# Performance work log

Measured on AMD Instinct MI355X. Metric: run time of the kernel, lower is better.

## Reference

```python
import jax, jax.numpy as jnp
import numpy as np

B, S, E, H, F, V = 4, 2048, 1024, 16, 4096, 32000
D = E // H  # head_dim = 64
LN_EPS = 1e-5


def layer_norm(x, g, b):
    mu = jnp.mean(x, axis=-1, keepdims=True)
    var = jnp.mean(jnp.square(x - mu), axis=-1, keepdims=True)
    return (x - mu) * jax.lax.rsqrt(var + LN_EPS) * g + b


def setup_inputs() -> dict:
    key = jax.random.key(0)
    ks = jax.random.split(key, 12)
    s = 0.02
    return {
        "input_ids": jax.random.randint(ks[0], (B, S), 0, V),
        "attention_mask": jnp.ones((B, S), dtype=jnp.int32),
        "emb_table": jax.random.normal(ks[1], (V, E), jnp.float32) * s,
        "Wq": jax.random.normal(ks[2], (E, E), jnp.float32) * s,
        "bq": jnp.zeros((E,), jnp.float32),
        "Wk": jax.random.normal(ks[3], (E, E), jnp.float32) * s,
        "bk": jnp.zeros((E,), jnp.float32),
        "Wv": jax.random.normal(ks[4], (E, E), jnp.float32) * s,
        "bv": jnp.zeros((E,), jnp.float32),
        "Wo": jax.random.normal(ks[5], (E, E), jnp.float32) * s,
        "bo": jnp.zeros((E,), jnp.float32),
        "ln_g": jnp.ones((E,), jnp.float32),
        "ln_b": jnp.zeros((E,), jnp.float32),
        "W1": jax.random.normal(ks[6], (E, F), jnp.float32) * s,
        "b1": jnp.zeros((F,), jnp.float32),
        "W2": jax.random.normal(ks[7], (F, E), jnp.float32) * s,
        "b2": jnp.zeros((E,), jnp.float32),
        "Wp": jax.random.normal(ks[8], (E, 3), jnp.float32) * s,
        "bp": jnp.zeros((3,), jnp.float32),
    }


def reference(input_ids, attention_mask, emb_table, Wq, bq, Wk, bk, Wv, bv,
              Wo, bo, ln_g, ln_b, W1, b1, W2, b2, Wp, bp):
    b, s = input_ids.shape
    x = emb_table[input_ids]                                  # [B,S,E]
    q = (x @ Wq + bq).reshape(b, s, H, D).transpose(0, 2, 1, 3)  # [B,H,S,D]
    k = (x @ Wk + bk).reshape(b, s, H, D).transpose(0, 2, 1, 3)
    v = (x @ Wv + bv).reshape(b, s, H, D).transpose(0, 2, 1, 3)
    scores = jnp.einsum('bhqd,bhkd->bhqk', q, k) / jnp.sqrt(jnp.float32(D))
    mask = attention_mask[:, None, None, :]                   # [B,1,1,S]
    scores = jnp.where(mask == 0, -jnp.inf, scores)
    attn = jax.nn.softmax(scores, axis=-1)
    ctx = jnp.einsum('bhqk,bhkd->bhqd', attn, v)              # [B,H,S,D]
    ctx = ctx.transpose(0, 2, 1, 3).reshape(b, s, E)
    ctx = ctx @ Wo + bo
    h = layer_norm(ctx + x, ln_g, ln_b)
    ff = jax.nn.gelu(h @ W1 + b1, approximate=False) @ W2 + b2
    logits = ff @ Wp + bp                                     # [B,S,3]
    return logits.mean(axis=1)                                # [B,3]
```

## Files before the change

### kernel.cpp

```cpp
#include <hip/hip_runtime.h>
#include <hip/hip_bf16.h>
#include <math.h>

#define BB 4
#define SS 2048
#define EE 1024
#define HH 16
#define DD 64
#define FF 4096

typedef unsigned short u16;
typedef unsigned int u32;
typedef __bf16 bf16x8 __attribute__((ext_vector_type(8)));
typedef float f32x4 __attribute__((ext_vector_type(4)));

static __device__ __forceinline__ float gelu_exact(float v){
  return 0.5f * v * (1.0f + erff(v * 0.70710678118654752f));
}

static __device__ __forceinline__ u16 f2bf(float f){
  union { float f; u32 u; } x; x.f = f;
  u32 r = x.u + 0x7FFFu + ((x.u >> 16) & 1u);
  return (u16)(r >> 16);
}
static __device__ __forceinline__ u16 f2bf_hw(float f){
  union { __bf16 b; u16 u; } c; c.b = (__bf16)f; return c.u;
}
static __device__ __forceinline__ void unpack2(u32 u, float& lo, float& hi){
  union { u32 u; float f; } a, b;
  a.u = u << 16; b.u = u & 0xFFFF0000u;
  lo = a.f; hi = b.f;
}

#define GLOAD_LDS16(g, l) \
  __builtin_amdgcn_global_load_lds((const __attribute__((address_space(1))) void*)(g), \
      (__attribute__((address_space(3))) void*)(l), 16, 0, 0)

__global__ __launch_bounds__(256) void embed_kernel(const int* __restrict__ ids,
    const float* __restrict__ emb, float* __restrict__ xf, u16* __restrict__ xbf){
  int row = blockIdx.x;
  int id  = ids[row];
  float4 v = ((const float4*)(emb + (size_t)id * EE))[threadIdx.x];
  ((float4*)(xf + (size_t)row * EE))[threadIdx.x] = v;
  ushort4 u; u.x = f2bf(v.x); u.y = f2bf(v.y); u.z = f2bf(v.z); u.w = f2bf(v.w);
  ((ushort4*)(xbf + (size_t)row * EE))[threadIdx.x] = u;
}

__global__ __launch_bounds__(256) void prep_weights(const float* __restrict__ Wq,
    const float* __restrict__ Wk, const float* __restrict__ Wv,
    const float* __restrict__ Wo, const float* __restrict__ W1, u16* __restrict__ WT){
  __shared__ float tile[32][33];
  int bid = blockIdx.x;
  const float* W; u16* dst; int N, n0, k0;
  if (bid < 4096){
    W = W1; dst = WT + (size_t)4 * EE * EE; N = FF;
    n0 = (bid & 127) * 32; k0 = (bid >> 7) * 32;
  } else {
    int idx = bid - 4096;
    int which = idx >> 10, t = idx & 1023;
    W = (which == 0) ? Wq : (which == 1) ? Wk : (which == 2) ? Wv : Wo;
    dst = WT + (size_t)which * EE * EE; N = EE;
    n0 = (t & 31) * 32; k0 = (t >> 5) * 32;
  }
  int tx = threadIdx.x & 31, ty = threadIdx.x >> 5;
  #pragma unroll
  for (int i = 0; i < 4; i++)
    tile[ty + 8*i][tx] = W[(size_t)(k0 + ty + 8*i) * N + n0 + tx];
  __syncthreads();
  #pragma unroll
  for (int i = 0; i < 4; i++)
    dst[(size_t)(n0 + ty + 8*i) * EE + k0 + tx] = f2bf(tile[tx][ty + 8*i]);
}

template<int MODE>
__global__ __launch_bounds__(256) void gemm_mfma(const u16* __restrict__ A,
    const u16* __restrict__ WT, const float* __restrict__ bias,
    const float* __restrict__ biasB, const float* __restrict__ biasC,
    u16* __restrict__ C, float* __restrict__ gsum, int M, int N, int K){
  __shared__ __attribute__((aligned(16))) u16 As[2][128 * 32];
  __shared__ __attribute__((aligned(16))) u16 Bs[2][128 * 32];

  const int tid = threadIdx.x;
  const int l = tid & 63, w = tid >> 6;
  const int lm = l & 15, lq = l >> 4;
  const int wm = (w >> 1) * 64, wn = (w & 1) * 64;

  const int nwg = gridDim.x * gridDim.y;
  const int bid = blockIdx.y * gridDim.x + blockIdx.x;
  const int q8  = nwg >> 3;
  const int lin = (bid & 7) * q8 + (bid >> 3);
  const int bx  = lin % gridDim.x;
  const int by  = lin / gridDim.x;
  const int r0 = by * 128, c0 = bx * 128;

  const int srow0 = w * 32 + (l >> 2);
  const int scol  = (l & 3) * 8;
  const u16* Ab = A  + (size_t)(r0 + srow0) * K + scol;
  const u16* Bb = WT + (size_t)(c0 + srow0) * K + scol;
  const int sbase = (w * 2) * 512;

  f32x4 acc[4][4];
  const f32x4 zero = {0.f, 0.f, 0.f, 0.f};
  #pragma unroll
  for (int mi = 0; mi < 4; mi++)
    #pragma unroll
    for (int ni = 0; ni < 4; ni++) acc[mi][ni] = zero;

  GLOAD_LDS16(Ab,                  &As[0][sbase]);
  GLOAD_LDS16(Ab + (size_t)16 * K, &As[0][sbase + 512]);
  GLOAD_LDS16(Bb,                  &Bs[0][sbase]);
  GLOAD_LDS16(Bb + (size_t)16 * K, &Bs[0][sbase + 512]);
  __syncthreads();

  int p = 0;
  for (int k0 = 0; k0 < K; k0 += 32){
    if (k0 + 32 < K){
      const int pn = p ^ 1;
      GLOAD_LDS16(Ab + k0 + 32,                   &As[pn][sbase]);
      GLOAD_LDS16(Ab + (size_t)16 * K + k0 + 32,  &As[pn][sbase + 512]);
      GLOAD_LDS16(Bb + k0 + 32,                   &Bs[pn][sbase]);
      GLOAD_LDS16(Bb + (size_t)16 * K + k0 + 32,  &Bs[pn][sbase + 512]);
    }

    bf16x8 af[4], bfr[4];
    #pragma unroll
    for (int mi = 0; mi < 4; mi++)
      af[mi] = *(const bf16x8*)&As[p][(wm + mi*16 + lm) * 32 + lq * 8];
    #pragma unroll
    for (int ni = 0; ni < 4; ni++)
      bfr[ni] = *(const bf16x8*)&Bs[p][(wn + ni*16 + lm) * 32 + lq * 8];
    #pragma unroll
    for (int mi = 0; mi < 4; mi++)
      #pragma unroll
      for (int ni = 0; ni < 4; ni++)
        acc[mi][ni] = __builtin_amdgcn_mfma_f32_16x16x32_bf16(af[mi], bfr[ni], acc[mi][ni], 0, 0, 0);

    __syncthreads();
    p ^= 1;
  }

  if constexpr (MODE == 0){
    #pragma unroll
    for (int ni = 0; ni < 4; ni++){
      int col = c0 + wn + ni*16 + lm;
      float bcol = bias[col];
      #pragma unroll
      for (int mi = 0; mi < 4; mi++){
        #pragma unroll
        for (int r = 0; r < 4; r++){
          int row = r0 + wm + mi*16 + lq*4 + r;
          C[(size_t)row * N + col] = f2bf(acc[mi][ni][r] + bcol);
        }
      }
    }
  } else if constexpr (MODE == 2){
    #pragma unroll
    for (int ni = 0; ni < 4; ni++){
      int col3 = c0 + wn + ni*16 + lm;
      int sel  = col3 >> 10;
      int colm = col3 & 1023;
      const float* bp_ = (sel == 0) ? bias : ((sel == 1) ? biasB : biasC);
      float bcol = bp_[colm];
      u16* dst = C + (size_t)sel * ((size_t)M * N);
      #pragma unroll
      for (int mi = 0; mi < 4; mi++){
        #pragma unroll
        for (int r = 0; r < 4; r++){
          int row = r0 + wm + mi*16 + lq*4 + r;
          dst[(size_t)row * N + colm] = f2bf(acc[mi][ni][r] + bcol);
        }
      }
    }
  } else {
    const int batch = r0 >> 11;
    #pragma unroll
    for (int ni = 0; ni < 4; ni++){
      int col = c0 + wn + ni*16 + lm;
      float bcol = bias[col];
      float cs = 0.f;
      #pragma unroll
      for (int mi = 0; mi < 4; mi++)
        #pragma unroll
        for (int r = 0; r < 4; r++)
          cs += gelu_exact(acc[mi][ni][r] + bcol);
      cs += __shfl_xor(cs, 16, 64);
      cs += __shfl_xor(cs, 32, 64);
      if (lq == 0) atomicAdd(&gsum[(size_t)batch * N + col], cs);
    }
  }
}

__global__ __launch_bounds__(256, 2) void attn_mfma(const u16* __restrict__ q,
    const u16* __restrict__ k, const u16* __restrict__ v,
    const int* __restrict__ mask, u16* __restrict__ ctx){
  const int bid = blockIdx.y * gridDim.x + blockIdx.x;
  const int lin = (bid & 7) * 128 + (bid >> 3);
  const int qb  = lin & 15, bh = lin >> 4;
  const int b = bh >> 4, h = bh & 15;
  const int q0 = qb * 128;
  const int tid = threadIdx.x;
  const int w = tid >> 6, l = tid & 63, lm = l & 15, lq = l >> 4;

  __shared__ __attribute__((aligned(16))) u16 smem[128 * 72];
  __shared__ __attribute__((aligned(16))) float mb[64];
  u16* Kt = smem;
  u16* Vt = smem + 64 * 72;

  bf16x8 aq[2][2];
  #pragma unroll
  for (int mg = 0; mg < 2; mg++){
    const u16* qrow = q + (size_t)(b*SS + q0 + w*32 + mg*16 + lm) * EE + h*DD + lq*8;
    aq[mg][0] = *(const bf16x8*)qrow;
    aq[mg][1] = *(const bf16x8*)(qrow + 32);
  }

  f32x4 occ[2][4];
  const f32x4 zero = {0.f,0.f,0.f,0.f};
  #pragma unroll
  for (int mg = 0; mg < 2; mg++)
    #pragma unroll
    for (int mi = 0; mi < 4; mi++) occ[mg][mi] = zero;
  float l_part[2] = {0.f, 0.f};

  const int kkey = tid >> 2, kc16 = (tid & 3) * 16;
  const u16* kbase = k + (size_t)(b*SS + kkey) * EE + h*DD + kc16;
  const int kp = tid & 31, vd0 = (tid >> 5) * 8;
  const u16* vbase0 = v + (size_t)(b*SS + 2*kp) * EE + h*DD + vd0;
  const u16* vbase1 = vbase0 + EE;

  uint4 kr0 = *(const uint4*)(kbase);
  uint4 kr1 = *(const uint4*)(kbase + 8);
  uint4 vr0 = *(const uint4*)(vbase0);
  uint4 vr1 = *(const uint4*)(vbase1);
  float mreg = 0.f;
  if (tid < 64) mreg = (mask[b*SS + tid] != 0) ? 0.f : -1e30f;

  const float SCALE_LOG2E = 0.125f * 1.4426950408889634f;

  for (int t0 = 0; t0 < SS; t0 += 64){
    *(uint4*)&Kt[kkey*72 + kc16]     = kr0;
    *(uint4*)&Kt[kkey*72 + kc16 + 8] = kr1;
    {
      union { uint4 u; u16 s[8]; } va, vb;
      va.u = vr0; vb.u = vr1;
      #pragma unroll
      for (int i = 0; i < 8; i++){
        u32 pk = (u32)va.s[i] | ((u32)vb.s[i] << 16);
        *(u32*)&Vt[(vd0 + i)*72 + 2*kp] = pk;
      }
    }
    if (tid < 64) mb[tid] = mreg;
    __syncthreads();

    if (t0 + 64 < SS){
      kr0 = *(const uint4*)(kbase + (size_t)(t0 + 64) * EE);
      kr1 = *(const uint4*)(kbase + (size_t)(t0 + 64) * EE + 8);
      vr0 = *(const uint4*)(vbase0 + (size_t)(t0 + 64) * EE);
      vr1 = *(const uint4*)(vbase1 + (size_t)(t0 + 64) * EE);
      if (tid < 64) mreg = (mask[b*SS + t0 + 64 + tid] != 0) ? 0.f : -1e30f;
    }

    bf16x8 pb[2][2];
    #pragma unroll
    for (int mg = 0; mg < 2; mg++){
      float lp = 0.f;
      #pragma unroll
      for (int h2 = 0; h2 < 2; h2++){
        u32 pk[2][2];
        #pragma unroll
        for (int np = 0; np < 2; np++){
          int ni = h2*2 + np;
          bf16x8 kf0 = *(const bf16x8*)&Kt[(ni*16 + lm)*72 + lq*8];
          bf16x8 kf1 = *(const bf16x8*)&Kt[(ni*16 + lm)*72 + 32 + lq*8];
          f32x4 sc = zero;
          __builtin_amdgcn_s_setprio(1);
          sc = __builtin_amdgcn_mfma_f32_16x16x32_bf16(kf0, aq[mg][0], sc, 0, 0, 0);
          sc = __builtin_amdgcn_mfma_f32_16x16x32_bf16(kf1, aq[mg][1], sc, 0, 0, 0);
          __builtin_amdgcn_s_setprio(0);
          f32x4 mbv = *(const f32x4*)&mb[ni*16 + lq*4];
          float p[4];
          #pragma unroll
          for (int r = 0; r < 4; r++){
            float s = fminf(fmaf(sc[r], SCALE_LOG2E, mbv[r]), 80.f);
            p[r] = __builtin_amdgcn_exp2f(s);
            lp += p[r];
          }
          pk[np][0] = (u32)f2bf_hw(p[0]) | ((u32)f2bf_hw(p[1]) << 16);
          pk[np][1] = (u32)f2bf_hw(p[2]) | ((u32)f2bf_hw(p[3]) << 16);
        }
        int srcA = lm + 16*((2*lq)     & 3);
        int srcB = lm + 16*((2*lq + 1) & 3);
        u32 x0 = (u32)__shfl((int)pk[0][0], srcA, 64);
        u32 x1 = (u32)__shfl((int)pk[0][1], srcA, 64);
        u32 x2 = (u32)__shfl((int)pk[0][0], srcB, 64);
        u32 x3 = (u32)__shfl((int)pk[0][1], srcB, 64);
        u32 y0 = (u32)__shfl((int)pk[1][0], srcA, 64);
        u32 y1 = (u32)__shfl((int)pk[1][1], srcA, 64);
        u32 y2 = (u32)__shfl((int)pk[1][0], srcB, 64);
        u32 y3 = (u32)__shfl((int)pk[1][1], srcB, 64);
        bool lo = (lq < 2);
        union { u32 u[4]; bf16x8 v; } pu;
        pu.u[0] = lo ? x0 : y0;
        pu.u[1] = lo ? x1 : y1;
        pu.u[2] = lo ? x2 : y2;
        pu.u[3] = lo ? x3 : y3;
        pb[mg][h2] = pu.v;
      }
      l_part[mg] += lp;
    }

    __builtin_amdgcn_s_setprio(1);
    #pragma unroll
    for (int mi = 0; mi < 4; mi++){
      bf16x8 vb0 = *(const bf16x8*)&Vt[(mi*16 + lm)*72 + lq*8];
      bf16x8 vb1 = *(const bf16x8*)&Vt[(mi*16 + lm)*72 + 32 + lq*8];
      #pragma unroll
      for (int mg = 0; mg < 2; mg++){
        occ[mg][mi] = __builtin_amdgcn_mfma_f32_16x16x32_bf16(vb0, pb[mg][0], occ[mg][mi], 0, 0, 0);
        occ[mg][mi] = __builtin_amdgcn_mfma_f32_16x16x32_bf16(vb1, pb[mg][1], occ[mg][mi], 0, 0, 0);
      }
    }
    __builtin_amdgcn_s_setprio(0);
    __syncthreads();
  }

  #pragma unroll
  for (int mg = 0; mg < 2; mg++){
    float s = l_part[mg];
    s += __shfl_xor(s, 16, 64);
    s += __shfl_xor(s, 32, 64);
    float inv = 1.f / s;
    #pragma unroll
    for (int mi = 0; mi < 4; mi++){
      ushort4 o;
      o.x = f2bf(occ[mg][mi][0] * inv);
      o.y = f2bf(occ[mg][mi][1] * inv);
      o.z = f2bf(occ[mg][mi][2] * inv);
      o.w = f2bf(occ[mg][mi][3] * inv);
      *(ushort4*)&smem[(w*32 + mg*16 + lm)*72 + mi*16 + lq*4] = o;
    }
  }
  __syncthreads();
  {
    const int row = tid >> 1, half = tid & 1;
    u16* dst = ctx + (size_t)(b*SS + q0 + row) * EE + h*DD + half*32;
    const u16* src = &smem[row*72 + half*32];
    #pragma unroll
    for (int jj = 0; jj < 4; jj++)
      *(uint4*)(dst + jj*8) = *(const uint4*)(src + jj*8);
  }
}

__global__ __launch_bounds__(256) void ln_kernel(const u16* __restrict__ c2,
    const float* __restrict__ x, const float* __restrict__ g,
    const float* __restrict__ bta, u16* __restrict__ h){
  int row = blockIdx.x, tid = threadIdx.x;
  uint2 cu = ((const uint2*)(c2 + (size_t)row * EE))[tid];
  float c0,c1,c2f,c3;
  unpack2(cu.x, c0, c1); unpack2(cu.y, c2f, c3);
  float4 xv = ((const float4*)(x + (size_t)row * EE))[tid];
  float4 y = make_float4(c0+xv.x, c1+xv.y, c2f+xv.z, c3+xv.w);
  float s  = y.x + y.y + y.z + y.w;
  float ss = y.x*y.x + y.y*y.y + y.z*y.z + y.w*y.w;
  #pragma unroll
  for (int off=32; off; off>>=1){
    s  += __shfl_xor(s,  off, 64);
    ss += __shfl_xor(ss, off, 64);
  }
  __shared__ float rs[4], rss[4];
  int w = tid >> 6;
  if ((tid & 63) == 0){ rs[w] = s; rss[w] = ss; }
  __syncthreads();
  float tot  = rs[0]+rs[1]+rs[2]+rs[3];
  float tots = rss[0]+rss[1]+rss[2]+rss[3];
  float mu  = tot  * (1.f/EE);
  float var = tots * (1.f/EE) - mu*mu;
  float inv = rsqrtf(var + 1e-5f);
  float4 gv = ((const float4*)g)[tid];
  float4 bv = ((const float4*)bta)[tid];
  ushort4 ou;
  ou.x = f2bf((y.x-mu)*inv*gv.x + bv.x);
  ou.y = f2bf((y.y-mu)*inv*gv.y + bv.y);
  ou.z = f2bf((y.z-mu)*inv*gv.z + bv.z);
  ou.w = f2bf((y.w-mu)*inv*gv.w + bv.w);
  ((ushort4*)(h + (size_t)row * EE))[tid] = ou;
}

__global__ __launch_bounds__(256) void w2wp_kernel(const float* __restrict__ W2,
    const float* __restrict__ Wp, float* __restrict__ W2Wp){
  int f0 = blockIdx.x * 8;
  int tid = threadIdx.x;
  int e0 = tid * 4;
  float wp[4][3];
  #pragma unroll
  for (int t = 0; t < 4; t++)
    #pragma unroll
    for (int j = 0; j < 3; j++) wp[t][j] = Wp[(e0 + t)*3 + j];
  __shared__ float red[3][4];
  for (int i = 0; i < 8; i++){
    int f = f0 + i;
    float4 wv = ((const float4*)(W2 + (size_t)f * EE))[tid];
    float w4[4] = {wv.x, wv.y, wv.z, wv.w};
    float p[3] = {0.f, 0.f, 0.f};
    #pragma unroll
    for (int t = 0; t < 4; t++)
      #pragma unroll
      for (int j = 0; j < 3; j++) p[j] += w4[t] * wp[t][j];
    #pragma unroll
    for (int j = 0; j < 3; j++){
      float sj = p[j];
      #pragma unroll
      for (int off = 32; off; off >>= 1) sj += __shfl_xor(sj, off, 64);
      if ((tid & 63) == 0) red[j][tid >> 6] = sj;
    }
    __syncthreads();
    if (tid < 3) W2Wp[f*3 + tid] = red[tid][0] + red[tid][1] + red[tid][2] + red[tid][3];
    __syncthreads();
  }
}

__global__ __launch_bounds__(256) void out_final(const float* __restrict__ gsum,
    const float* __restrict__ W2Wp, const float* __restrict__ b2,
    const float* __restrict__ Wp, const float* __restrict__ bp, float* __restrict__ out){
  int tid = threadIdx.x;
  float part[4][3];
  #pragma unroll
  for (int b = 0; b < 4; b++)
    #pragma unroll
    for (int j = 0; j < 3; j++) part[b][j] = 0.f;
  for (int f = tid; f < FF; f += 256){
    float w0 = W2Wp[f*3], w1 = W2Wp[f*3+1], w2v = W2Wp[f*3+2];
    #pragma unroll
    for (int b = 0; b < 4; b++){
      float g = gsum[b*FF + f] * (1.f/SS);
      part[b][0] += g * w0; part[b][1] += g * w1; part[b][2] += g * w2v;
    }
  }
  float bb[3] = {0.f, 0.f, 0.f};
  for (int e = tid; e < EE; e += 256){
    float bv = b2[e];
    bb[0] += bv * Wp[e*3]; bb[1] += bv * Wp[e*3+1]; bb[2] += bv * Wp[e*3+2];
  }
  __shared__ float red[15][4];
  int lane = tid & 63, w = tid >> 6;
  #pragma unroll
  for (int b = 0; b < 4; b++)
    #pragma unroll
    for (int j = 0; j < 3; j++){
      float s = part[b][j];
      #pragma unroll
      for (int off = 32; off; off >>= 1) s += __shfl_xor(s, off, 64);
      if (lane == 0) red[b*3 + j][w] = s;
    }
  #pragma unroll
  for (int j = 0; j < 3; j++){
    float s = bb[j];
    #pragma unroll
    for (int off = 32; off; off >>= 1) s += __shfl_xor(s, off, 64);
    if (lane == 0) red[12 + j][w] = s;
  }
  __syncthreads();
  if (tid < 12){
    int j = tid % 3;
    float s  = red[tid][0] + red[tid][1] + red[tid][2] + red[tid][3];
    float bj = red[12+j][0] + red[12+j][1] + red[12+j][2] + red[12+j][3];
    out[tid] = s + bj + bp[j];
  }
}

extern "C" void kernel_launch(void* const* d_in, const int* in_sizes, int n_in,
                              void* d_out, int out_size, void* d_ws, size_t ws_size,
                              hipStream_t stream) {
  const int M = BB * SS;
  const int* ids  = (const int*)d_in[0];
  const int* mask = (const int*)d_in[1];
  const float* emb = (const float*)d_in[2];
  const float* Wq = (const float*)d_in[3];  const float* bq = (const float*)d_in[4];
  const float* Wk = (const float*)d_in[5];  const float* bk = (const float*)d_in[6];
  const float* Wv = (const float*)d_in[7];  const float* bv = (const float*)d_in[8];
  const float* Wo = (const float*)d_in[9];  const float* bo = (const float*)d_in[10];
  const float* lg = (const float*)d_in[11]; const float* lb = (const float*)d_in[12];
  const float* W1 = (const float*)d_in[13]; const float* b1 = (const float*)d_in[14];
  const float* W2 = (const float*)d_in[15]; const float* b2 = (const float*)d_in[16];
  const float* Wp = (const float*)d_in[17]; const float* bp = (const float*)d_in[18];

  char* base = (char*)d_ws;
  const size_t SLOTF = (size_t)M * EE;
  float* xf   = (float*)base;
  u16*  xbf   = (u16*)(base + SLOTF*4);
  u16*  qbf   = (u16*)(base + SLOTF*6);
  u16*  kbf   = (u16*)(base + SLOTF*8);
  u16*  vbf   = (u16*)(base + SLOTF*10);
  u16*  ctxbf = (u16*)(base + SLOTF*12);
  u16*  c2bf  = qbf;
  u16*  hbf   = kbf;
  u16*  WqT   = (u16*)(base + SLOTF*14);
  u16*  W1T   = WqT + (size_t)4*EE*EE;
  float* gsum = (float*)(W1T + (size_t)FF*EE);
  float* w2wp = gsum + BB*FF;

  hipMemsetAsync(gsum, 0, BB*FF*sizeof(float), stream);

  embed_kernel<<<M, 256, 0, stream>>>(ids, emb, xf, xbf);

  prep_weights<<<8192, 256, 0, stream>>>(Wq, Wk, Wv, Wo, W1, WqT);
  w2wp_kernel<<<FF/8, 256, 0, stream>>>(W2, Wp, w2wp);

  gemm_mfma<2><<<dim3(3*EE/128, M/128), 256, 0, stream>>>(
      xbf, WqT, bq, bk, bv, qbf, nullptr, M, EE, EE);

  attn_mfma<<<dim3(SS/128, BB*HH), 256, 0, stream>>>(qbf, kbf, vbf, mask, ctxbf);

  gemm_mfma<0><<<dim3(EE/128, M/128), 256, 0, stream>>>(
      ctxbf, WqT + (size_t)3*EE*EE, bo, nullptr, nullptr, c2bf, nullptr, M, EE, EE);

  ln_kernel<<<M, 256, 0, stream>>>(c2bf, xf, lg, lb, hbf);

  gemm_mfma<1><<<dim3(FF/128, M/128), 256, 0, stream>>>(
      hbf, W1T, b1, nullptr, nullptr, nullptr, gsum, M, FF, EE);

  out_final<<<1, 256, 0, stream>>>(gsum, w2wp, b2, Wp, bp, (float*)d_out);
}
```

Measured before the change: 613.1 us.

## Add 256x256 swizzled pipelined GEMM, precompute mask bias, remove attention P shuffles

Adds a new 512-thread GEMM kernel with 256x256 tiles, 64-wide K steps, XOR-swizzled LDS and a staged prefetch interleaved with MFMA groups, and uses it for the QKV projection and the FFN1+GELU reduction. The larger tiles are meant to raise data reuse per LDS load and cut global traffic, at the cost of more registers and LDS per block and fewer blocks in flight. Attention now reads a precomputed float mask bias from global memory instead of staging it through LDS. It also permutes the V layout in LDS so the probability fragments can feed the second MFMA directly, removing eight cross-lane shuffles per step.

Measured after the change: 593.5 us. -3.2%, faster.

```diff
diff --git a/kernel.cpp b/kernel.cpp
--- a/kernel.cpp
+++ b/kernel.cpp
@@ -35,6 +35,12 @@
 #define GLOAD_LDS16(g, l) \
   __builtin_amdgcn_global_load_lds((const __attribute__((address_space(1))) void*)(g), \
       (__attribute__((address_space(3))) void*)(l), 16, 0, 0)
+
+static __device__ __forceinline__ void blockbar(){
+  asm volatile("" ::: "memory");
+  __builtin_amdgcn_s_barrier();
+  asm volatile("" ::: "memory");
+}
 
 __global__ __launch_bounds__(256) void embed_kernel(const int* __restrict__ ids,
     const float* __restrict__ emb, float* __restrict__ xf, u16* __restrict__ xbf){
@@ -44,6 +50,12 @@
   ((float4*)(xf + (size_t)row * EE))[threadIdx.x] = v;
   ushort4 u; u.x = f2bf(v.x); u.y = f2bf(v.y); u.z = f2bf(v.z); u.w = f2bf(v.w);
   ((ushort4*)(xbf + (size_t)row * EE))[threadIdx.x] = u;
+}
+
+__global__ __launch_bounds__(256) void mask_prep(const int* __restrict__ mask,
+    float* __restrict__ mbias){
+  int i = blockIdx.x * 256 + threadIdx.x;
+  mbias[i] = (mask[i] != 0) ? 0.f : -1e30f;
 }
 
 __global__ __launch_bounds__(256) void prep_weights(const float* __restrict__ Wq,
@@ -121,7 +133,6 @@
       GLOAD_LDS16(Bb + k0 + 32,                   &Bs[pn][sbase]);
       GLOAD_LDS16(Bb + (size_t)16 * K + k0 + 32,  &Bs[pn][sbase + 512]);
     }
-
     bf16x8 af[4], bfr[4];
     #pragma unroll
     for (int mi = 0; mi < 4; mi++)
@@ -134,7 +145,6 @@
       #pragma unroll
       for (int ni = 0; ni < 4; ni++)
         acc[mi][ni] = __builtin_amdgcn_mfma_f32_16x16x32_bf16(af[mi], bfr[ni], acc[mi][ni], 0, 0, 0);
-
     __syncthreads();
     p ^= 1;
   }
@@ -153,7 +163,135 @@
         }
       }
     }
-  } else if constexpr (MODE == 2){
+  }
+}
+
+template<int MODE>
+__global__ __launch_bounds__(512, 2) void gemm256(const u16* __restrict__ A,
+    const u16* __restrict__ WT, const float* __restrict__ bias,
+    const float* __restrict__ biasB, const float* __restrict__ biasC,
+    u16* __restrict__ C, float* __restrict__ gsum, int M, int N, int K){
+  __shared__ __attribute__((aligned(16))) u16 As[2 * 256 * 64];
+  __shared__ __attribute__((aligned(16))) u16 Bs[2 * 256 * 64];
+
+  const int tid = threadIdx.x;
+  const int w = tid >> 6, l = tid & 63;
+  const int lm = l & 15, lq = l >> 4;
+  const int wm = (w >> 2) * 128, wn = (w & 3) * 64;
+
+  const int nwg = gridDim.x * gridDim.y;
+  const int bid = blockIdx.y * gridDim.x + blockIdx.x;
+  const int lin = (bid & 7) * (nwg >> 3) + (bid >> 3);
+  const int bx = lin % gridDim.x, by = lin / gridDim.x;
+  const int r0 = by * 256, c0 = bx * 256;
+
+  const int NT = K >> 6;
+  const int arow = w * 8 + (l >> 3);
+  const int acol = ((l & 7) ^ (l >> 3)) * 8;
+  const u16* Ag = A  + (size_t)(r0 + arow) * K + acol;
+  const u16* Bg = WT + (size_t)(c0 + arow) * K + acol;
+  const int dstw = w * 512;
+
+#define STG_A(p_, kt_, g_) GLOAD_LDS16(Ag + (size_t)((g_)*64) * K + (kt_)*64, &As[(p_)*16384 + (g_)*4096 + dstw])
+#define STG_B(p_, kt_, g_) GLOAD_LDS16(Bg + (size_t)((g_)*64) * K + (kt_)*64, &Bs[(p_)*16384 + (g_)*4096 + dstw])
+
+  const int rsw = (lm & 7) << 3;
+#define RD_A(p_, mi_, kk_) (*(const bf16x8*)&As[(p_)*16384 + (wm + (mi_)*16 + lm)*64 + (((kk_)*32 + lq*8) ^ rsw)])
+#define RD_B(p_, ni_, kk_) (*(const bf16x8*)&Bs[(p_)*16384 + (wn + (ni_)*16 + lm)*64 + (((kk_)*32 + lq*8) ^ rsw)])
+
+  f32x4 acc[8][4];
+  const f32x4 zero = {0.f, 0.f, 0.f, 0.f};
+  #pragma unroll
+  for (int mi = 0; mi < 8; mi++)
+    #pragma unroll
+    for (int ni = 0; ni < 4; ni++) acc[mi][ni] = zero;
+
+  #pragma unroll
+  for (int g = 0; g < 4; g++){ STG_A(0, 0, g); STG_B(0, 0, g); }
+  #pragma unroll
+  for (int g = 0; g < 4; g++){ STG_A(1, 1, g); STG_B(1, 1, g); }
+  asm volatile("s_waitcnt vmcnt(8)" ::: "memory");
+  __builtin_amdgcn_s_barrier();
+  asm volatile("" ::: "memory");
+
+  bf16x8 a0[4][2], a1[4][2], b0[2][2], b1[2][2];
+
+  for (int t = 0; t < NT; ++t){
+    const int p = t & 1;
+    const int s = t + 2;
+    const bool st = (s < NT);
+
+    #pragma unroll
+    for (int mi = 0; mi < 4; mi++){ a0[mi][0] = RD_A(p, mi, 0); a0[mi][1] = RD_A(p, mi, 1); }
+    #pragma unroll
+    for (int ni = 0; ni < 2; ni++){ b0[ni][0] = RD_B(p, ni, 0); b0[ni][1] = RD_B(p, ni, 1); }
+    blockbar();
+    __builtin_amdgcn_s_setprio(1);
+    #pragma unroll
+    for (int kk = 0; kk < 2; kk++)
+      #pragma unroll
+      for (int mi = 0; mi < 4; mi++)
+        #pragma unroll
+        for (int ni = 0; ni < 2; ni++)
+          acc[mi][ni] = __builtin_amdgcn_mfma_f32_16x16x32_bf16(a0[mi][kk], b0[ni][kk], acc[mi][ni], 0, 0, 0);
+    __builtin_amdgcn_s_setprio(0);
+    blockbar();
+
+    #pragma unroll
+    for (int ni = 0; ni < 2; ni++){ b1[ni][0] = RD_B(p, ni + 2, 0); b1[ni][1] = RD_B(p, ni + 2, 1); }
+    if (st){ STG_A(p, s, 0); STG_A(p, s, 2); }
+    blockbar();
+    __builtin_amdgcn_s_setprio(1);
+    #pragma unroll
+    for (int kk = 0; kk < 2; kk++)
+      #pragma unroll
+      for (int mi = 0; mi < 4; mi++)
+        #pragma unroll
+        for (int ni = 0; ni < 2; ni++)
+          acc[mi][ni + 2] = __builtin_amdgcn_mfma_f32_16x16x32_bf16(a0[mi][kk], b1[ni][kk], acc[mi][ni + 2], 0, 0, 0);
+    __builtin_amdgcn_s_setprio(0);
+    blockbar();
+
+    #pragma unroll
+    for (int mi = 0; mi < 4; mi++){ a1[mi][0] = RD_A(p, mi + 4, 0); a1[mi][1] = RD_A(p, mi + 4, 1); }
+    if (st){ STG_B(p, s, 0); STG_B(p, s, 1); }
+    blockbar();
+    __builtin_amdgcn_s_setprio(1);
+    #pragma unroll
+    for (int kk = 0; kk < 2; kk++)
+      #pragma unroll
+      for (int mi = 0; mi < 4; mi++)
+        #pragma unroll
+        for (int ni = 0; ni < 2; ni++)
+          acc[mi + 4][ni] = __builtin_amdgcn_mfma_f32_16x16x32_bf16(a1[mi][kk], b0[ni][kk], acc[mi + 4][ni], 0, 0, 0);
+    __builtin_amdgcn_s_setprio(0);
+    blockbar();
+
+    if (st){ STG_A(p, s, 1); STG_A(p, s, 3); STG_B(p, s, 2); STG_B(p, s, 3); }
+    blockbar();
+    __builtin_amdgcn_s_setprio(1);
+    #pragma unroll
+    for (int kk = 0; kk < 2; kk++)
+      #pragma unroll
+      for (int mi = 0; mi < 4; mi++)
+        #pragma unroll
+        for (int ni = 0; ni < 2; ni++)
+          acc[mi + 4][ni + 2] = __builtin_amdgcn_mfma_f32_16x16x32_bf16(a1[mi][kk], b1[ni][kk], acc[mi + 4][ni + 2], 0, 0, 0);
+    __builtin_amdgcn_s_setprio(0);
+    if (t + 1 < NT){
+      if (st) asm volatile("s_waitcnt vmcnt(8)" ::: "memory");
+      else    asm volatile("s_waitcnt vmcnt(0)" ::: "memory");
+      __builtin_amdgcn_s_barrier();
+      asm volatile("" ::: "memory");
+    }
+  }
+
+#undef STG_A
+#undef STG_B
+#undef RD_A
+#undef RD_B
+
+  if constexpr (MODE == 2){
     #pragma unroll
     for (int ni = 0; ni < 4; ni++){
       int col3 = c0 + wn + ni*16 + lm;
@@ -161,25 +299,25 @@
       int colm = col3 & 1023;
       const float* bp_ = (sel == 0) ? bias : ((sel == 1) ? biasB : biasC);
       float bcol = bp_[colm];
-      u16* dst = C + (size_t)sel * ((size_t)M * N);
-      #pragma unroll
-      for (int mi = 0; mi < 4; mi++){
+      u16* dst = C + (size_t)sel * ((size_t)M * 1024);
+      #pragma unroll
+      for (int mi = 0; mi < 8; mi++){
         #pragma unroll
         for (int r = 0; r < 4; r++){
           int row = r0 + wm + mi*16 + lq*4 + r;
-          dst[(size_t)row * N + colm] = f2bf(acc[mi][ni][r] + bcol);
+          dst[(size_t)row * 1024 + colm] = f2bf(acc[mi][ni][r] + bcol);
         }
       }
     }
   } else {
-    const int batch = r0 >> 11;
+    const int batch = (r0 + wm) >> 11;
     #pragma unroll
     for (int ni = 0; ni < 4; ni++){
       int col = c0 + wn + ni*16 + lm;
       float bcol = bias[col];
       float cs = 0.f;
       #pragma unroll
-      for (int mi = 0; mi < 4; mi++)
+      for (int mi = 0; mi < 8; mi++)
         #pragma unroll
         for (int r = 0; r < 4; r++)
           cs += gelu_exact(acc[mi][ni][r] + bcol);
@@ -192,7 +330,7 @@
 
 __global__ __launch_bounds__(256, 2) void attn_mfma(const u16* __restrict__ q,
     const u16* __restrict__ k, const u16* __restrict__ v,
-    const int* __restrict__ mask, u16* __restrict__ ctx){
+    const float* __restrict__ mbias, u16* __restrict__ ctx){
   const int bid = blockIdx.y * gridDim.x + blockIdx.x;
   const int lin = (bid & 7) * 128 + (bid >> 3);
   const int qb  = lin & 15, bh = lin >> 4;
@@ -202,7 +340,6 @@
   const int w = tid >> 6, l = tid & 63, lm = l & 15, lq = l >> 4;
 
   __shared__ __attribute__((aligned(16))) u16 smem[128 * 72];
-  __shared__ __attribute__((aligned(16))) float mb[64];
   u16* Kt = smem;
   u16* Vt = smem + 64 * 72;
 
@@ -225,6 +362,7 @@
   const int kkey = tid >> 2, kc16 = (tid & 3) * 16;
   const u16* kbase = k + (size_t)(b*SS + kkey) * EE + h*DD + kc16;
   const int kp = tid & 31, vd0 = (tid >> 5) * 8;
+  const int vslot = ((kp >> 1) & 3) * 8 + ((kp >> 3) & 1) * 4 + (kp & 1) * 2 + (kp >> 4) * 32;
   const u16* vbase0 = v + (size_t)(b*SS + 2*kp) * EE + h*DD + vd0;
   const u16* vbase1 = vbase0 + EE;
 
@@ -232,10 +370,9 @@
   uint4 kr1 = *(const uint4*)(kbase + 8);
   uint4 vr0 = *(const uint4*)(vbase0);
   uint4 vr1 = *(const uint4*)(vbase1);
-  float mreg = 0.f;
-  if (tid < 64) mreg = (mask[b*SS + tid] != 0) ? 0.f : -1e30f;
 
   const float SCALE_LOG2E = 0.125f * 1.4426950408889634f;
+  const float* mrow = mbias + (size_t)b * SS;
 
   for (int t0 = 0; t0 < SS; t0 += 64){
     *(uint4*)&Kt[kkey*72 + kc16]     = kr0;
@@ -246,10 +383,9 @@
       #pragma unroll
       for (int i = 0; i < 8; i++){
         u32 pk = (u32)va.s[i] | ((u32)vb.s[i] << 16);
-        *(u32*)&Vt[(vd0 + i)*72 + 2*kp] = pk;
+        *(u32*)&Vt[(vd0 + i)*72 + vslot] = pk;
       }
     }
-    if (tid < 64) mb[tid] = mreg;
     __syncthreads();
 
     if (t0 + 64 < SS){
@@ -257,8 +393,12 @@
       kr1 = *(const uint4*)(kbase + (size_t)(t0 + 64) * EE + 8);
       vr0 = *(const uint4*)(vbase0 + (size_t)(t0 + 64) * EE);
       vr1 = *(const uint4*)(vbase1 + (size_t)(t0 + 64) * EE);
-      if (tid < 64) mreg = (mask[b*SS + t0 + 64 + tid] != 0) ? 0.f : -1e30f;
-    }
+    }
+
+    f32x4 mt[4];
+    #pragma unroll
+    for (int ni = 0; ni < 4; ni++)
+      mt[ni] = *(const f32x4*)&mrow[t0 + ni*16 + lq*4];
 
     bf16x8 pb[2][2];
     #pragma unroll
@@ -266,7 +406,7 @@
       float lp = 0.f;
       #pragma unroll
       for (int h2 = 0; h2 < 2; h2++){
-        u32 pk[2][2];
+        u32 pk_[2][2];
         #pragma unroll
         for (int np = 0; np < 2; np++){
           int ni = h2*2 + np;
@@ -277,33 +417,21 @@
           sc = __builtin_amdgcn_mfma_f32_16x16x32_bf16(kf0, aq[mg][0], sc, 0, 0, 0);
           sc = __builtin_amdgcn_mfma_f32_16x16x32_bf16(kf1, aq[mg][1], sc, 0, 0, 0);
           __builtin_amdgcn_s_setprio(0);
-          f32x4 mbv = *(const f32x4*)&mb[ni*16 + lq*4];
           float p[4];
           #pragma unroll
           for (int r = 0; r < 4; r++){
-            float s = fminf(fmaf(sc[r], SCALE_LOG2E, mbv[r]), 80.f);
+            float s = fminf(fmaf(sc[r], SCALE_LOG2E, mt[ni][r]), 80.f);
             p[r] = __builtin_amdgcn_exp2f(s);
             lp += p[r];
           }
-          pk[np][0] = (u32)f2bf_hw(p[0]) | ((u32)f2bf_hw(p[1]) << 16);
-          pk[np][1] = (u32)f2bf_hw(p[2]) | ((u32)f2bf_hw(p[3]) << 16);
+          pk_[np][0] = (u32)f2bf_hw(p[0]) | ((u32)f2bf_hw(p[1]) << 16);
+          pk_[np][1] = (u32)f2bf_hw(p[2]) | ((u32)f2bf_hw(p[3]) << 16);
         }
-        int srcA = lm + 16*((2*lq)     & 3);
-        int srcB = lm + 16*((2*lq + 1) & 3);
-        u32 x0 = (u32)__shfl((int)pk[0][0], srcA, 64);
-        u32 x1 = (u32)__shfl((int)pk[0][1], srcA, 64);
-        u32 x2 = (u32)__shfl((int)pk[0][0], srcB, 64);
-        u32 x3 = (u32)__shfl((int)pk[0][1], srcB, 64);
-        u32 y0 = (u32)__shfl((int)pk[1][0], srcA, 64);
-        u32 y1 = (u32)__shfl((int)pk[1][1], srcA, 64);
-        u32 y2 = (u32)__shfl((int)pk[1][0], srcB, 64);
-        u32 y3 = (u32)__shfl((int)pk[1][1], srcB, 64);
-        bool lo = (lq < 2);
         union { u32 u[4]; bf16x8 v; } pu;
-        pu.u[0] = lo ? x0 : y0;
-        pu.u[1] = lo ? x1 : y1;
-        pu.u[2] = lo ? x2 : y2;
-        pu.u[3] = lo ? x3 : y3;
+        pu.u[0] = pk_[0][0];
+        pu.u[1] = pk_[0][1];
+        pu.u[2] = pk_[1][0];
+        pu.u[3] = pk_[1][1];
         pb[mg][h2] = pu.v;
       }
       l_part[mg] += lp;
@@ -498,25 +626,27 @@
   u16*  W1T   = WqT + (size_t)4*EE*EE;
   float* gsum = (float*)(W1T + (size_t)FF*EE);
   float* w2wp = gsum + BB*FF;
+  float* mbias = w2wp + FF*3;
 
   hipMemsetAsync(gsum, 0, BB*FF*sizeof(float), stream);
 
   embed_kernel<<<M, 256, 0, stream>>>(ids, emb, xf, xbf);
+  mask_prep<<<BB*SS/256, 256, 0, stream>>>(mask, mbias);
 
   prep_weights<<<8192, 256, 0, stream>>>(Wq, Wk, Wv, Wo, W1, WqT);
   w2wp_kernel<<<FF/8, 256, 0, stream>>>(W2, Wp, w2wp);
 
-  gemm_mfma<2><<<dim3(3*EE/128, M/128), 256, 0, stream>>>(
+  gemm256<2><<<dim3(3*EE/256, M/256), 512, 0, stream>>>(
       xbf, WqT, bq, bk, bv, qbf, nullptr, M, EE, EE);
 
-  attn_mfma<<<dim3(SS/128, BB*HH), 256, 0, stream>>>(qbf, kbf, vbf, mask, ctxbf);
+  attn_mfma<<<dim3(SS/128, BB*HH), 256, 0, stream>>>(qbf, kbf, vbf, mbias, ctxbf);
 
   gemm_mfma<0><<<dim3(EE/128, M/128), 256, 0, stream>>>(
       ctxbf, WqT + (size_t)3*EE*EE, bo, nullptr, nullptr, c2bf, nullptr, M, EE, EE);
 
   ln_kernel<<<M, 256, 0, stream>>>(c2bf, xf, lg, lb, hbf);
 
-  gemm_mfma<1><<<dim3(FF/128, M/128), 256, 0, stream>>>(
+  gemm256<1><<<dim3(FF/256, M/256), 512, 0, stream>>>(
       hbf, W1T, b1, nullptr, nullptr, nullptr, gsum, M, FF, EE);
 
   out_final<<<1, 256, 0, stream>>>(gsum, w2wp, b2, Wp, bp, (float*)d_out);
```
